# Optimization experiments

Hardware: AMD Instinct MI355X
Metric: run time of the kernel (lower is better)

## Reference

```python
import jax, jax.numpy as jnp
import numpy as np

N_NODES = 8192
D_FEAT = 128
R_BITS = 8      # rows per band
B_BANDS = 64    # number of LSH bands
D_THRESH = 0.25 # cosine-distance threshold from LSH(z, d=0.25, ...)


def setup_inputs() -> dict:
    key = jax.random.key(0)
    k1, k2, k3 = jax.random.split(key, 3)
    z = jax.random.normal(k1, (N_NODES, D_FEAT), dtype=jnp.float32)
    # random hyperplanes for signed-projection LSH: r*b = 512 planes
    H = jax.random.normal(k2, (D_FEAT, R_BITS * B_BANDS), dtype=jnp.float32)
    edge_index = jax.random.randint(k3, (2, N_NODES * 16), 0, N_NODES, dtype=jnp.int64)
    return {"z": z, "H": H, "edge_index": edge_index}


def reference(z, H, edge_index):
    # edge_index is unused by forward_all (kept for signature fidelity).
    N = z.shape[0]
    # --- hyperplane LSH signatures ---
    bits = (z @ H) > 0                              # [N, r*b] bool
    bits = bits.reshape(N, B_BANDS, R_BITS)         # [N, b, r]
    powers = (2 ** jnp.arange(R_BITS)).astype(jnp.int32)
    codes = jnp.sum(bits.astype(jnp.int32) * powers, axis=-1)  # [N, b] band hash codes

    # --- candidate pairs: collide in at least one band (OR over bands) ---
    def band_or(mask, c):  # c: [N] codes for one band
        return mask | (c[:, None] == c[None, :]), None
    collide, _ = jax.lax.scan(band_or, jnp.zeros((N, N), dtype=bool), codes.T)

    # --- exact cosine similarity on candidates ---
    zn = z / jnp.linalg.norm(z, axis=1, keepdims=True)
    S = zn @ zn.T                                   # [N, N] cosine similarity
    dist = 1.0 - S                                  # cosine distance

    eye = jnp.eye(N, dtype=bool)
    # pairs kept by LSH: colliding, within distance threshold, off-diagonal
    keep = collide & (dist < D_THRESH) & (~eye)
    # adjacency[v1, v2] = 1 - dist = cos_sim (sigmoid=True path); identity on diagonal
    A = jnp.where(keep, S, 0.0) + eye.astype(S.dtype)
    return A
```

## Files before the change

kernel.cpp:

```cpp
#include <hip/hip_runtime.h>
#include <hip/hip_bf16.h>

#define N_NODES 8192
#define D_FEAT 128

typedef __bf16 bf16x8 __attribute__((ext_vector_type(8)));
typedef float f32x4 __attribute__((ext_vector_type(4)));
typedef unsigned long long u64;

__device__ __attribute__((noinline)) bool lsh_collide(
    const float* __restrict__ z, const float* __restrict__ H, int i, int j) {
  for (int b = 0; b < 64; ++b) {
    unsigned ci = 0, cj = 0;
    for (int bit = 0; bit < 8; ++bit) {
      int col = b * 8 + bit;
      float di = 0.f, dj = 0.f;
      for (int k = 0; k < D_FEAT; ++k) {
        float h = H[(size_t)k * 512 + col];
        di += z[(size_t)i * D_FEAT + k] * h;
        dj += z[(size_t)j * D_FEAT + k] * h;
      }
      if (di > 0.f) ci |= (1u << bit);
      if (dj > 0.f) cj |= (1u << bit);
    }
    if (ci == cj) return true;
  }
  return false;
}

__device__ __forceinline__ unsigned pack_bf16x2(float x, float y) {
  __hip_bfloat16 bx = __float2bfloat16(x), by = __float2bfloat16(y);
  return (unsigned)(*(unsigned short*)&bx) |
         ((unsigned)(*(unsigned short*)&by) << 16);
}

__global__ __launch_bounds__(256, 2) void sim_kernel(const float* __restrict__ z,
                                                     const float* __restrict__ H,
                                                     float* __restrict__ out) {
  __shared__ __align__(16) unsigned char smem_raw[65536];
  unsigned short (*As)[128] = (unsigned short (*)[128])smem_raw;
  unsigned short (*Bs)[128] = (unsigned short (*)[128])(smem_raw + 32768);
  float* fS = (float*)smem_raw;

  int tid = threadIdx.x;
  int bm = blockIdx.x, bn = blockIdx.y;

  {
    int row = tid >> 1, half = tid & 1;
#pragma unroll
    for (int pass = 0; pass < 2; ++pass) {
      int gr = (pass ? bn : bm) * 128 + row;
      const float4* src = (const float4*)(z + (size_t)gr * D_FEAT + half * 64);
      float4 v[16];
#pragma unroll
      for (int c = 0; c < 16; ++c) v[c] = src[c];
      float ss = 0.f;
#pragma unroll
      for (int c = 0; c < 16; ++c)
        ss += v[c].x * v[c].x + v[c].y * v[c].y + v[c].z * v[c].z + v[c].w * v[c].w;
      ss += __shfl_xor(ss, 1);
      float inv = rsqrtf(ss);
      unsigned short (*T)[128] = pass ? Bs : As;
#pragma unroll
      for (int c = 0; c < 8; ++c) {
        float4 a = v[2 * c], b = v[2 * c + 1];
        uint4 o;
        o.x = pack_bf16x2(a.x * inv, a.y * inv);
        o.y = pack_bf16x2(a.z * inv, a.w * inv);
        o.z = pack_bf16x2(b.x * inv, b.y * inv);
        o.w = pack_bf16x2(b.z * inv, b.w * inv);
        int cg = half * 8 + c;
        ((uint4*)&T[row][0])[cg ^ (row & 15)] = o;
      }
    }
  }
  __syncthreads();

  int wv = tid >> 6, lane = tid & 63;
  int wm = (wv >> 1) * 64, wn = (wv & 1) * 64;
  int m16 = lane & 15, g = lane >> 4;

  f32x4 acc[4][4] = {};

#pragma unroll
  for (int kc = 0; kc < 4; ++kc) {
    bf16x8 fa[4], fb[4];
    int chunk = kc * 4 + g;
    int cs = (chunk ^ m16) * 8;
#pragma unroll
    for (int t = 0; t < 4; ++t) {
      fa[t] = *(const bf16x8*)&As[wm + t * 16 + m16][cs];
      fb[t] = *(const bf16x8*)&Bs[wn + t * 16 + m16][cs];
    }
#pragma unroll
    for (int tm = 0; tm < 4; ++tm)
#pragma unroll
      for (int tn = 0; tn < 4; ++tn)
        acc[tm][tn] = __builtin_amdgcn_mfma_f32_16x16x32_bf16(fa[tm], fb[tn], acc[tm][tn], 0, 0, 0);
  }

  __syncthreads();

#pragma unroll
  for (int tm = 0; tm < 4; ++tm) {
#pragma unroll
    for (int tn = 0; tn < 4; ++tn) {
      int col = wn + tn * 16 + m16;
      int j = bn * 128 + col;
      f32x4 c = acc[tm][tn];
#pragma unroll
      for (int r = 0; r < 4; ++r) {
        int row = wm + tm * 16 + g * 4 + r;
        int i = bm * 128 + row;
        float s = c[r];
        float val = 0.0f;
        if (i == j) {
          val = 1.0f;
        } else if (s > 0.75f) {
          if (lsh_collide(z, H, i, j)) val = s;
        }
        fS[row * 128 + ((((col >> 2) ^ (row & 31)) << 2) | (col & 3))] = val;
      }
    }
  }
  __syncthreads();

#pragma unroll
  for (int r = 0; r < 16; ++r) {
    int slot = tid + 256 * r;
    int row = slot >> 5, chunk = slot & 31;
    float4 v = *(const float4*)&fS[row * 128 + ((chunk ^ (row & 31)) << 2)];
    *(float4*)&out[(size_t)(bm * 128 + row) * N_NODES + bn * 128 + chunk * 4] = v;
  }
}

extern "C" void kernel_launch(void* const* d_in, const int* in_sizes, int n_in,
                              void* d_out, int out_size, void* d_ws, size_t ws_size,
                              hipStream_t stream) {
  const float* z = (const float*)d_in[0];
  const float* H = (const float*)d_in[1];
  float* out = (float*)d_out;
  (void)d_ws; (void)ws_size;

  sim_kernel<<<dim3(64, 64), 256, 0, stream>>>(z, H, out);
}
```

Baseline: 300.6 us.

## Persist blocks over eight row tiles reusing staged column tile, per-wave epilogue staging

Launches 512 blocks, each of which stages one normalized column tile once and then loops over eight row tiles, so the B-tile load and normalization are not repeated. The epilogue now stages results per wave in 16-row slabs with only a waitcnt fence instead of full-block syncthreads, and writes rows straight to global memory. Block-wide barriers are replaced with explicit lgkmcnt waits plus s_barrier. The cost is a smaller grid (512 blocks of 256 threads) with less latency hiding between the store-heavy epilogue and compute, and a serialized per-block loop.

```diff
diff --git a/kernel.cpp b/kernel.cpp
--- a/kernel.cpp
+++ b/kernel.cpp
@@ -6,7 +6,13 @@
 
 typedef __bf16 bf16x8 __attribute__((ext_vector_type(8)));
 typedef float f32x4 __attribute__((ext_vector_type(4)));
-typedef unsigned long long u64;
+
+__device__ __forceinline__ void lgkm_barrier() {
+  asm volatile("s_waitcnt lgkmcnt(0)\n\ts_barrier" ::: "memory");
+}
+__device__ __forceinline__ void lgkm_fence() {
+  asm volatile("s_waitcnt lgkmcnt(0)" ::: "memory");
+}
 
 __device__ __attribute__((noinline)) bool lsh_collide(
     const float* __restrict__ z, const float* __restrict__ H, int i, int j) {
@@ -34,6 +40,31 @@
          ((unsigned)(*(unsigned short*)&by) << 16);
 }
 
+__device__ __forceinline__ void stage_tile(const float* __restrict__ z, int blk,
+                                           unsigned short (*T)[128], int tid) {
+  int row = tid >> 1, half = tid & 1;
+  const float4* src = (const float4*)(z + (size_t)(blk * 128 + row) * D_FEAT + half * 64);
+  float4 v[16];
+#pragma unroll
+  for (int c = 0; c < 16; ++c) v[c] = src[c];
+  float ss = 0.f;
+#pragma unroll
+  for (int c = 0; c < 16; ++c)
+    ss += v[c].x * v[c].x + v[c].y * v[c].y + v[c].z * v[c].z + v[c].w * v[c].w;
+  ss += __shfl_xor(ss, 1);
+  float inv = rsqrtf(ss);
+#pragma unroll
+  for (int c = 0; c < 8; ++c) {
+    float4 a = v[2 * c], b = v[2 * c + 1];
+    uint4 o;
+    o.x = pack_bf16x2(a.x * inv, a.y * inv);
+    o.y = pack_bf16x2(a.z * inv, a.w * inv);
+    o.z = pack_bf16x2(b.x * inv, b.y * inv);
+    o.w = pack_bf16x2(b.z * inv, b.w * inv);
+    ((uint4*)&T[row][0])[(half * 8 + c) ^ (row & 15)] = o;
+  }
+}
+
 __global__ __launch_bounds__(256, 2) void sim_kernel(const float* __restrict__ z,
                                                      const float* __restrict__ H,
                                                      float* __restrict__ out) {
@@ -43,94 +74,75 @@
   float* fS = (float*)smem_raw;
 
   int tid = threadIdx.x;
-  int bm = blockIdx.x, bn = blockIdx.y;
-
-  {
-    int row = tid >> 1, half = tid & 1;
-#pragma unroll
-    for (int pass = 0; pass < 2; ++pass) {
-      int gr = (pass ? bn : bm) * 128 + row;
-      const float4* src = (const float4*)(z + (size_t)gr * D_FEAT + half * 64);
-      float4 v[16];
-#pragma unroll
-      for (int c = 0; c < 16; ++c) v[c] = src[c];
-      float ss = 0.f;
-#pragma unroll
-      for (int c = 0; c < 16; ++c)
-        ss += v[c].x * v[c].x + v[c].y * v[c].y + v[c].z * v[c].z + v[c].w * v[c].w;
-      ss += __shfl_xor(ss, 1);
-      float inv = rsqrtf(ss);
-      unsigned short (*T)[128] = pass ? Bs : As;
-#pragma unroll
-      for (int c = 0; c < 8; ++c) {
-        float4 a = v[2 * c], b = v[2 * c + 1];
-        uint4 o;
-        o.x = pack_bf16x2(a.x * inv, a.y * inv);
-        o.y = pack_bf16x2(a.z * inv, a.w * inv);
-        o.z = pack_bf16x2(b.x * inv, b.y * inv);
-        o.w = pack_bf16x2(b.z * inv, b.w * inv);
-        int cg = half * 8 + c;
-        ((uint4*)&T[row][0])[cg ^ (row & 15)] = o;
-      }
-    }
-  }
-  __syncthreads();
+  int b = (int)blockIdx.x;
+  int bn = b & 63;
+  int bm0 = b >> 6;
 
   int wv = tid >> 6, lane = tid & 63;
   int wm = (wv >> 1) * 64, wn = (wv & 1) * 64;
   int m16 = lane & 15, g = lane >> 4;
+  float* fSw = fS + wv * 2048;
 
-  f32x4 acc[4][4] = {};
+  stage_tile(z, bn, Bs, tid);
+
+  for (int t = 0; t < 8; ++t) {
+    int bm = bm0 * 8 + t;
+
+    lgkm_barrier();
+    stage_tile(z, bm, As, tid);
+    lgkm_barrier();
+
+    f32x4 acc[4][4] = {};
+#pragma unroll
+    for (int kc = 0; kc < 4; ++kc) {
+      bf16x8 fa[4], fb[4];
+      int chunk = kc * 4 + g;
+      int cs = (chunk ^ m16) * 8;
+#pragma unroll
+      for (int tt = 0; tt < 4; ++tt) {
+        fa[tt] = *(const bf16x8*)&As[wm + tt * 16 + m16][cs];
+        fb[tt] = *(const bf16x8*)&Bs[wn + tt * 16 + m16][cs];
+      }
+#pragma unroll
+      for (int tm = 0; tm < 4; ++tm)
+#pragma unroll
+        for (int tn = 0; tn < 4; ++tn)
+          acc[tm][tn] = __builtin_amdgcn_mfma_f32_16x16x32_bf16(fa[tm], fb[tn], acc[tm][tn], 0, 0, 0);
+    }
+
+    lgkm_barrier();
 
 #pragma unroll
-  for (int kc = 0; kc < 4; ++kc) {
-    bf16x8 fa[4], fb[4];
-    int chunk = kc * 4 + g;
-    int cs = (chunk ^ m16) * 8;
+    for (int tm = 0; tm < 4; ++tm) {
+      float* slab = fSw + (tm & 1) * 1024;
 #pragma unroll
-    for (int t = 0; t < 4; ++t) {
-      fa[t] = *(const bf16x8*)&As[wm + t * 16 + m16][cs];
-      fb[t] = *(const bf16x8*)&Bs[wn + t * 16 + m16][cs];
-    }
+      for (int tn = 0; tn < 4; ++tn) {
+        int colq = tn * 16 + m16;
+        int j = bn * 128 + wn + colq;
+        f32x4 c = acc[tm][tn];
 #pragma unroll
-    for (int tm = 0; tm < 4; ++tm)
+        for (int r = 0; r < 4; ++r) {
+          int rs = g * 4 + r;
+          int i = bm * 128 + wm + tm * 16 + rs;
+          float s = c[r];
+          float val = 0.0f;
+          if (i == j) {
+            val = 1.0f;
+          } else if (s > 0.75f) {
+            if (lsh_collide(z, H, i, j)) val = s;
+          }
+          slab[rs * 64 + (((colq >> 2) ^ rs) << 2) + (colq & 3)] = val;
+        }
+      }
+      lgkm_fence();
 #pragma unroll
-      for (int tn = 0; tn < 4; ++tn)
-        acc[tm][tn] = __builtin_amdgcn_mfma_f32_16x16x32_bf16(fa[tm], fb[tn], acc[tm][tn], 0, 0, 0);
-  }
-
-  __syncthreads();
-
-#pragma unroll
-  for (int tm = 0; tm < 4; ++tm) {
-#pragma unroll
-    for (int tn = 0; tn < 4; ++tn) {
-      int col = wn + tn * 16 + m16;
-      int j = bn * 128 + col;
-      f32x4 c = acc[tm][tn];
-#pragma unroll
-      for (int r = 0; r < 4; ++r) {
-        int row = wm + tm * 16 + g * 4 + r;
-        int i = bm * 128 + row;
-        float s = c[r];
-        float val = 0.0f;
-        if (i == j) {
-          val = 1.0f;
-        } else if (s > 0.75f) {
-          if (lsh_collide(z, H, i, j)) val = s;
-        }
-        fS[row * 128 + ((((col >> 2) ^ (row & 31)) << 2) | (col & 3))] = val;
+      for (int it = 0; it < 4; ++it) {
+        int rs = it * 4 + g;
+        f32x4 v = *(const f32x4*)&slab[rs * 64 + ((m16 ^ rs) << 2)];
+        int grow = bm * 128 + wm + tm * 16 + rs;
+        *(f32x4*)&out[(size_t)grow * N_NODES + bn * 128 + wn + m16 * 4] = v;
       }
     }
-  }
-  __syncthreads();
-
-#pragma unroll
-  for (int r = 0; r < 16; ++r) {
-    int slot = tid + 256 * r;
-    int row = slot >> 5, chunk = slot & 31;
-    float4 v = *(const float4*)&fS[row * 128 + ((chunk ^ (row & 31)) << 2)];
-    *(float4*)&out[(size_t)(bm * 128 + row) * N_NODES + bn * 128 + chunk * 4] = v;
   }
 }
 
@@ -142,5 +154,5 @@
   float* out = (float*)d_out;
   (void)d_ws; (void)ws_size;
 
-  sim_kernel<<<dim3(64, 64), 256, 0, stream>>>(z, H, out);
+  sim_kernel<<<512, 256, 0, stream>>>(z, H, out);
 }
```

After: 278.3 us. -7.4%, faster.
